# Optimization experiments

Hardware: AMD Instinct MI355X
Metric: run time of the kernel (lower is better)

## Reference

```python
import jax, jax.numpy as jnp
import numpy as np
from jax import lax


def setup_inputs() -> dict:
    key = jax.random.key(0)
    ks = jax.random.split(key, 6)
    B, T, F, C = 32, 256, 64, 16
    CO, P, S, K = 16, 64, 32, 4
    x = jax.random.normal(ks[0], (B, T, F, C), dtype=jnp.float32)
    static = jax.random.normal(ks[1], (B, S), dtype=jnp.float32)
    conv_w = jax.random.normal(ks[2], (F, CO, C, K), dtype=jnp.float32) * (1.0 / np.sqrt(C * K))
    conv_b = jax.random.normal(ks[3], (F, CO), dtype=jnp.float32) * 0.01
    W_p = jax.random.normal(ks[4], (F * C + S, P), dtype=jnp.float32) * (1.0 / np.sqrt(F * C + S))
    b_p = jax.random.normal(ks[5], (P,), dtype=jnp.float32) * 0.01
    return {"x": x, "static": static, "conv_w": conv_w, "conv_b": conv_b,
            "W_p": W_p, "b_p": b_p, "dilation": 2}


def _tpc_forward(x, static, conv_w, conv_b, W_p, b_p, dilation):
    B, T, F, C = x.shape
    _, CO, _, K = conv_w.shape
    left_pad = dilation * (K - 1)
    # --- feature-wise causal temporal conv as one grouped dilated conv ---
    # [B, T, F, C] -> [B, F*C, T]  (NCH layout)
    xr = x.transpose(0, 2, 3, 1).reshape(B, F * C, T)
    kr = conv_w.reshape(F * CO, C, K)  # groups = F
    y = lax.conv_general_dilated(
        xr, kr,
        window_strides=(1,),
        padding=[(left_pad, 0)],  # causal left padding
        rhs_dilation=(dilation,),
        dimension_numbers=("NCH", "OIH", "NCH"),
        feature_group_count=F,
    )  # [B, F*CO, T]
    temp_out = y.reshape(B, F, CO, T).transpose(0, 3, 1, 2) + conv_b[None, None, :, :]
    # --- pointwise branch on flattened features + static ---
    flat_x = x.reshape(B, T, F * C)
    static_rep = jnp.broadcast_to(static[:, None, :], (B, T, static.shape[-1]))
    point_in = jnp.concatenate([flat_x, static_rep], axis=-1)  # [B, T, F*C+S]
    point_out = point_in @ W_p + b_p  # [B, T, P]
    point_bcast = jnp.broadcast_to(point_out[:, :, None, :], (B, T, F, point_out.shape[-1]))
    # --- concat fusion + ReLU ---
    fused = jnp.concatenate([x, temp_out, point_bcast], axis=-1)
    return jax.nn.relu(fused)


def reference(x, static, conv_w, conv_b, W_p, b_p, dilation):
    return _tpc_forward(x, static, conv_w, conv_b, W_p, b_p, dilation)
```

## Files before the change

### kernel.cpp

```cpp
#include <hip/hip_runtime.h>

#define B_  32
#define T_  256
#define F_  64
#define C_  16
#define CO_ 16
#define P_  64
#define S_  32
#define K_  4
#define FC_ 1024
#define OUTC 96
#define TT  8
#define NS  14

__global__ __launch_bounds__(512, 4) void tpc_fused(
    const float* __restrict__ x, const float* __restrict__ stat,
    const float* __restrict__ cw, const float* __restrict__ cb,
    const float* __restrict__ Wp, const float* __restrict__ bp,
    float* __restrict__ out)
{
    __shared__ __align__(16) float xs[NS * FC_];
    __shared__ __align__(16) float u[4096];

    int tid = threadIdx.x;
    int blk = blockIdx.x;
    int b  = blk >> 5;
    int t0 = (blk & 31) * TT;

    #pragma unroll
    for (int it = 0; it < 7; ++it) {
        int v = it * 512 + tid;
        int slice = v >> 8;
        int pos   = v & 255;
        int tg = t0 - 6 + slice;
        float4 val = make_float4(0.f, 0.f, 0.f, 0.f);
        if (tg >= 0)
            val = *(const float4*)(x + ((size_t)(b * T_ + tg)) * FC_ + pos * 4);
        *(float4*)(xs + slice * FC_ + pos * 4) = val;
    }
    __syncthreads();

    {
        int p  = tid & 63;
        int ks = tid >> 6;
        float acc[TT];
        #pragma unroll
        for (int r = 0; r < TT; ++r) acc[r] = 0.f;
        int k0base = ks * 128;
        for (int kk = 0; kk < 128; kk += 4) {
            int k0 = k0base + kk;
            float w0 = Wp[(size_t)(k0 + 0) * P_ + p];
            float w1 = Wp[(size_t)(k0 + 1) * P_ + p];
            float w2 = Wp[(size_t)(k0 + 2) * P_ + p];
            float w3 = Wp[(size_t)(k0 + 3) * P_ + p];
            #pragma unroll
            for (int r = 0; r < TT; ++r) {
                float4 xv = *(const float4*)(xs + (6 + r) * FC_ + k0);
                acc[r] += xv.x * w0 + xv.y * w1 + xv.z * w2 + xv.w * w3;
            }
        }
        #pragma unroll
        for (int r = 0; r < TT; ++r)
            u[(ks * TT + r) * P_ + p] = acc[r];
    }
    __syncthreads();

    {
        int p = tid & 63;
        int r = tid >> 6;
        float s = bp[p];
        const float* wst = Wp + (size_t)FC_ * P_;
        #pragma unroll 8
        for (int si = 0; si < S_; ++si)
            s += stat[b * S_ + si] * wst[si * P_ + p];
        #pragma unroll
        for (int ks = 0; ks < 8; ++ks)
            s += u[(ks * TT + r) * P_ + p];
        __syncthreads();
        u[3072 + r * P_ + p] = fmaxf(s, 0.f);
    }
    __syncthreads();

    int co = tid & 15;
    int fh = tid >> 4;
    int p  = tid & 63;
    int fg = tid >> 6;

    #pragma unroll
    for (int half = 0; half < 2; ++half) {
        int f = half * 32 + fh;
        float w[64];
        const float4* wg = (const float4*)(cw + ((size_t)(f * CO_ + co)) * (C_ * K_));
        #pragma unroll
        for (int j = 0; j < 16; ++j) {
            float4 t4 = wg[j];
            w[4 * j + 0] = t4.x; w[4 * j + 1] = t4.y;
            w[4 * j + 2] = t4.z; w[4 * j + 3] = t4.w;
        }
        float bias = cb[f * CO_ + co];

        for (int tl = 0; tl < TT; ++tl) {
            float temp = bias;
            #pragma unroll
            for (int k = 0; k < K_; ++k) {
                const float* sp = xs + (tl + 2 * k) * FC_ + f * C_;
                #pragma unroll
                for (int c4 = 0; c4 < 4; ++c4) {
                    float4 xv = *(const float4*)(sp + c4 * 4);
                    temp += xv.x * w[(c4 * 4 + 0) * 4 + k];
                    temp += xv.y * w[(c4 * 4 + 1) * 4 + k];
                    temp += xv.z * w[(c4 * 4 + 2) * 4 + k];
                    temp += xv.w * w[(c4 * 4 + 3) * 4 + k];
                }
            }
            u[fh * OUTC + 16 + co] = fmaxf(temp, 0.f);
            u[fh * OUTC + co] = fmaxf(xs[(tl + 6) * FC_ + f * C_ + co], 0.f);
            float pvv = u[3072 + tl * P_ + p];
            #pragma unroll
            for (int fo = 0; fo < 4; ++fo)
                u[(fo * 8 + fg) * OUTC + 32 + p] = pvv;
            __syncthreads();
            {
                const float4* src = (const float4*)u;
                float4* dst = (float4*)(out + ((size_t)(b * T_ + t0 + tl)) * F_ * OUTC
                                        + half * 3072);
                dst[tid] = src[tid];
                if (tid < 256) dst[512 + tid] = src[512 + tid];
            }
            __syncthreads();
        }
    }
}

extern "C" void kernel_launch(void* const* d_in, const int* in_sizes, int n_in,
                              void* d_out, int out_size, void* d_ws, size_t ws_size,
                              hipStream_t stream) {
    const float* x    = (const float*)d_in[0];
    const float* stat = (const float*)d_in[1];
    const float* cw   = (const float*)d_in[2];
    const float* cb   = (const float*)d_in[3];
    const float* Wp   = (const float*)d_in[4];
    const float* bp   = (const float*)d_in[5];
    float* out = (float*)d_out;

    tpc_fused<<<1024, 512, 0, stream>>>(x, stat, cw, cb, Wp, bp, out);
}
```

Baseline: 278.2 us.

## Precompute conv outputs in registers and stream output rows with fewer barriers

The grouped conv for all 8 timesteps and both feature halves is now computed up front into registers. The output loop then writes each row directly to global memory: ReLU(x) straight from the shared x tile, the pointwise vector from a new small shared buffer, and only the conv part staged through a double-buffered shared slot. This replaces two block barriers per timestep per half with a single raw s_barrier per timestep. It also software-prefetches the next W_p rows in the pointwise GEMV. The cost is higher register pressure from holding 16 conv results alongside the 64 weights.

```diff
diff --git a/kernel.cpp b/kernel.cpp
--- a/kernel.cpp
+++ b/kernel.cpp
@@ -21,6 +21,7 @@
 {
     __shared__ __align__(16) float xs[NS * FC_];
     __shared__ __align__(16) float u[4096];
+    __shared__ __align__(16) float pv[TT * P_];
 
     int tid = threadIdx.x;
     int blk = blockIdx.x;
@@ -46,18 +47,23 @@
         float acc[TT];
         #pragma unroll
         for (int r = 0; r < TT; ++r) acc[r] = 0.f;
-        int k0base = ks * 128;
+        int k0 = ks * 128;
+        float w0 = Wp[(size_t)(k0 + 0) * P_ + p];
+        float w1 = Wp[(size_t)(k0 + 1) * P_ + p];
+        float w2 = Wp[(size_t)(k0 + 2) * P_ + p];
+        float w3 = Wp[(size_t)(k0 + 3) * P_ + p];
         for (int kk = 0; kk < 128; kk += 4) {
-            int k0 = k0base + kk;
-            float w0 = Wp[(size_t)(k0 + 0) * P_ + p];
-            float w1 = Wp[(size_t)(k0 + 1) * P_ + p];
-            float w2 = Wp[(size_t)(k0 + 2) * P_ + p];
-            float w3 = Wp[(size_t)(k0 + 3) * P_ + p];
+            int kn = k0 + kk + 4;
+            float n0 = Wp[(size_t)(kn + 0) * P_ + p];
+            float n1 = Wp[(size_t)(kn + 1) * P_ + p];
+            float n2 = Wp[(size_t)(kn + 2) * P_ + p];
+            float n3 = Wp[(size_t)(kn + 3) * P_ + p];
             #pragma unroll
             for (int r = 0; r < TT; ++r) {
-                float4 xv = *(const float4*)(xs + (6 + r) * FC_ + k0);
+                float4 xv = *(const float4*)(xs + (6 + r) * FC_ + k0 + kk);
                 acc[r] += xv.x * w0 + xv.y * w1 + xv.z * w2 + xv.w * w3;
             }
+            w0 = n0; w1 = n1; w2 = n2; w3 = n3;
         }
         #pragma unroll
         for (int r = 0; r < TT; ++r)
@@ -76,59 +82,76 @@
         #pragma unroll
         for (int ks = 0; ks < 8; ++ks)
             s += u[(ks * TT + r) * P_ + p];
-        __syncthreads();
-        u[3072 + r * P_ + p] = fmaxf(s, 0.f);
+        pv[r * P_ + p] = fmaxf(s, 0.f);
+    }
+
+    float cv[2][TT];
+    {
+        int co = tid & 15;
+        int fh = tid >> 4;
+        #pragma unroll
+        for (int half = 0; half < 2; ++half) {
+            int f = half * 32 + fh;
+            float w[64];
+            const float4* wg = (const float4*)(cw + ((size_t)(f * CO_ + co)) * (C_ * K_));
+            #pragma unroll
+            for (int j = 0; j < 16; ++j) {
+                float4 t4 = wg[j];
+                w[4 * j + 0] = t4.x; w[4 * j + 1] = t4.y;
+                w[4 * j + 2] = t4.z; w[4 * j + 3] = t4.w;
+            }
+            float bias = cb[f * CO_ + co];
+            #pragma unroll
+            for (int tl = 0; tl < TT; ++tl) {
+                float temp = bias;
+                #pragma unroll
+                for (int k = 0; k < K_; ++k) {
+                    const float* sp = xs + (tl + 2 * k) * FC_ + f * C_;
+                    #pragma unroll
+                    for (int c4 = 0; c4 < 4; ++c4) {
+                        float4 xv = *(const float4*)(sp + c4 * 4);
+                        temp += xv.x * w[(c4 * 4 + 0) * 4 + k];
+                        temp += xv.y * w[(c4 * 4 + 1) * 4 + k];
+                        temp += xv.z * w[(c4 * 4 + 2) * 4 + k];
+                        temp += xv.w * w[(c4 * 4 + 3) * 4 + k];
+                    }
+                }
+                cv[half][tl] = fmaxf(temp, 0.f);
+            }
+        }
     }
     __syncthreads();
 
-    int co = tid & 15;
-    int fh = tid >> 4;
-    int p  = tid & 63;
-    int fg = tid >> 6;
+    int fq  = tid >> 3;
+    int q   = tid & 7;
+    int qp  = tid & 15;
+    int fp0 = tid >> 4;
 
     #pragma unroll
-    for (int half = 0; half < 2; ++half) {
-        int f = half * 32 + fh;
-        float w[64];
-        const float4* wg = (const float4*)(cw + ((size_t)(f * CO_ + co)) * (C_ * K_));
-        #pragma unroll
-        for (int j = 0; j < 16; ++j) {
-            float4 t4 = wg[j];
-            w[4 * j + 0] = t4.x; w[4 * j + 1] = t4.y;
-            w[4 * j + 2] = t4.z; w[4 * j + 3] = t4.w;
+    for (int tl = 0; tl < TT; ++tl) {
+        float* cs = u + (tl & 1) * 1024;
+        cs[tid]       = cv[0][tl];
+        cs[tid + 512] = cv[1][tl];
+        asm volatile("s_waitcnt lgkmcnt(0)" ::: "memory");
+        __builtin_amdgcn_sched_barrier(0);
+        __builtin_amdgcn_s_barrier();
+        __builtin_amdgcn_sched_barrier(0);
+
+        float4* rowp = (float4*)(out + ((size_t)(b * T_ + t0 + tl)) * F_ * OUTC);
+
+        float4 v;
+        if (q < 4) {
+            float4 xv = *(const float4*)(xs + (6 + tl) * FC_ + fq * C_ + q * 4);
+            v = make_float4(fmaxf(xv.x, 0.f), fmaxf(xv.y, 0.f),
+                            fmaxf(xv.z, 0.f), fmaxf(xv.w, 0.f));
+        } else {
+            v = *(const float4*)(cs + fq * C_ + (q - 4) * 4);
         }
-        float bias = cb[f * CO_ + co];
+        rowp[fq * 24 + q] = v;
 
-        for (int tl = 0; tl < TT; ++tl) {
-            float temp = bias;
-            #pragma unroll
-            for (int k = 0; k < K_; ++k) {
-                const float* sp = xs + (tl + 2 * k) * FC_ + f * C_;
-                #pragma unroll
-                for (int c4 = 0; c4 < 4; ++c4) {
-                    float4 xv = *(const float4*)(sp + c4 * 4);
-                    temp += xv.x * w[(c4 * 4 + 0) * 4 + k];
-                    temp += xv.y * w[(c4 * 4 + 1) * 4 + k];
-                    temp += xv.z * w[(c4 * 4 + 2) * 4 + k];
-                    temp += xv.w * w[(c4 * 4 + 3) * 4 + k];
-                }
-            }
-            u[fh * OUTC + 16 + co] = fmaxf(temp, 0.f);
-            u[fh * OUTC + co] = fmaxf(xs[(tl + 6) * FC_ + f * C_ + co], 0.f);
-            float pvv = u[3072 + tl * P_ + p];
-            #pragma unroll
-            for (int fo = 0; fo < 4; ++fo)
-                u[(fo * 8 + fg) * OUTC + 32 + p] = pvv;
-            __syncthreads();
-            {
-                const float4* src = (const float4*)u;
-                float4* dst = (float4*)(out + ((size_t)(b * T_ + t0 + tl)) * F_ * OUTC
-                                        + half * 3072);
-                dst[tid] = src[tid];
-                if (tid < 256) dst[512 + tid] = src[512 + tid];
-            }
-            __syncthreads();
-        }
+        float4 pvv = *(const float4*)(pv + tl * P_ + qp * 4);
+        rowp[fp0 * 24 + 8 + qp]        = pvv;
+        rowp[(fp0 + 32) * 24 + 8 + qp] = pvv;
     }
 }
 
```

Result: slower. 412.7 us (+48.3%).
